# Kernel tuning notes

Hardware: AMD Instinct MI355X
Metric: run time of the kernel (lower is better)

Reference implementation:

```python
import jax, jax.numpy as jnp
import numpy as np

N_NODES = 50000
N_EDGES = 500000
HEADS = 4
OUT_CH = 64
POS_DIM = 16
IN_CH = 256
DIVERSITY_WEIGHT = 0.1
NEG_SLOPE = 0.2


def setup_inputs() -> dict:
    key = jax.random.key(0)
    k = jax.random.split(key, 6)
    x = jax.random.normal(k[0], (N_NODES, IN_CH + POS_DIM), dtype=jnp.float32)
    # edges with no self-loops by construction (col = row + nonzero offset mod N)
    row = jax.random.randint(k[1], (N_EDGES,), 0, N_NODES)
    off = jax.random.randint(k[2], (N_EDGES,), 1, N_NODES)
    col = (row + off) % N_NODES
    edge_index = jnp.stack([row, col]).astype(jnp.int64)
    lin_w = jax.random.normal(k[3], (HEADS * OUT_CH, IN_CH), dtype=jnp.float32) * (1.0 / np.sqrt(IN_CH))
    att = jax.random.normal(k[4], (1, HEADS, 2 * OUT_CH), dtype=jnp.float32) * 0.1
    pos_att = jax.random.normal(k[5], (1, HEADS, 2 * POS_DIM), dtype=jnp.float32) * 0.1
    bias = jnp.zeros((HEADS * OUT_CH,), dtype=jnp.float32)
    return {"x": x, "edge_index": edge_index, "lin_w": lin_w, "att": att,
            "pos_att": pos_att, "bias": bias}


def _forward(x, edge_index, lin_w, att, pos_att, bias):
    N = x.shape[0]
    H, C = HEADS, OUT_CH
    pos = x[:, -POS_DIM:]              # [N, P]
    content_feat = x[:, :-POS_DIM]     # [N, IN_CH]
    content = (content_feat @ lin_w.T).reshape(N, H, C)  # [N, H, C]

    # add self loops (input edges contain none)
    sl = jnp.arange(N)
    row = jnp.concatenate([edge_index[0], sl])  # [E+N]
    col = jnp.concatenate([edge_index[1], sl])

    # cat([x_i, x_j]) * att summed == per-node split logits, gathered per edge
    a_src = jnp.einsum('nhc,hc->nh', content, att[0, :, :C])   # [N, H]
    a_dst = jnp.einsum('nhc,hc->nh', content, att[0, :, C:])
    p_src = pos @ pos_att[0, :, :POS_DIM].T                    # [N, H]
    p_dst = pos @ pos_att[0, :, POS_DIM:].T

    alpha = a_src[row] + a_dst[col] + p_src[row] + p_dst[col]  # [E+N, H]
    alpha = jax.nn.leaky_relu(alpha, NEG_SLOPE)

    # segment softmax over destination node (row), PyG-style with +1e-16
    amax = jax.ops.segment_max(alpha, row, num_segments=N)
    alpha = jnp.exp(alpha - amax[row])
    denom = jax.ops.segment_sum(alpha, row, num_segments=N)
    alpha = alpha / (denom[row] + 1e-16)

    # attention-head diversity loss: pairwise cosine similarity of alpha columns
    norms = jnp.maximum(jnp.sqrt(jnp.sum(alpha * alpha, axis=0)), 1e-8)  # [H]
    an = alpha / norms
    corr = an.T @ an                                            # [H, H]
    corr = corr * (1.0 - jnp.eye(H, dtype=corr.dtype))          # zero diagonal
    diversity_loss = jnp.mean(corr) * DIVERSITY_WEIGHT

    msgs = content[col] * alpha[:, :, None]                     # [E+N, H, C]
    out = jax.ops.segment_sum(msgs, row, num_segments=N)        # [N, H, C]
    out = out.reshape(N, H * C) + bias
    return out, diversity_loss


def reference(x, edge_index, lin_w, att, pos_att, bias):
    return _forward(x, edge_index, lin_w, att, pos_att, bias)
```

## Files before the change

### kernel.cpp

```cpp
#include <hip/hip_runtime.h>
#include <math.h>

#define NN 50000
#define NE 500000
#define HH 4
#define CC 64
#define HC 256
#define PD 16
#define XD 272
#define NEG 0.2f
#define SB 1024
#define NBLK (NN / 4)

typedef _Float16 half4 __attribute__((ext_vector_type(4)));
typedef _Float16 half8 __attribute__((ext_vector_type(8)));
typedef float floatx4 __attribute__((ext_vector_type(4)));

__global__ void k_prep(const float* __restrict__ w, _Float16* __restrict__ wfrag,
                       int* __restrict__ counts, int* __restrict__ gcur) {
    int idx = blockIdx.x * blockDim.x + threadIdx.x;
    if (idx < NN) counts[idx] = 0;
    if (idx == NN) *gcur = 0;
    int j = idx & 7, lane = (idx >> 3) & 63, nt = (idx >> 9) & 3;
    int wv = (idx >> 11) & 3, kt = idx >> 13;
    int n = wv * 64 + nt * 16 + (lane & 15);
    int k = kt * 32 + (lane >> 4) * 8 + j;
    wfrag[idx] = (_Float16)w[(size_t)n * 256 + k];
}

__global__ __launch_bounds__(256) void k_gemm(const float* __restrict__ x,
                                              const _Float16* __restrict__ wfrag,
                                              const float* __restrict__ att,
                                              const float* __restrict__ patt,
                                              _Float16* __restrict__ content,
                                              float* __restrict__ ssrc,
                                              float* __restrict__ sdst) {
    const int tid = threadIdx.x;
    const int wv = tid >> 6, lane = tid & 63;
    const int nb = blockIdx.x * 64;
    const int m16 = lane & 15, q = lane >> 4;

    floatx4 acc[4][4];
#pragma unroll
    for (int mt = 0; mt < 4; mt++)
#pragma unroll
        for (int nt = 0; nt < 4; nt++) acc[mt][nt] = (floatx4){0.f, 0.f, 0.f, 0.f};

    const float* xr[4];
#pragma unroll
    for (int mt = 0; mt < 4; mt++) {
        int node = nb + mt * 16 + m16;
        if (node >= NN) node = NN - 1;
        xr[mt] = &x[(size_t)node * XD + q * 8];
    }

#pragma unroll
    for (int kt = 0; kt < 8; kt++) {
        half8 bf[4];
#pragma unroll
        for (int nt = 0; nt < 4; nt++)
            bf[nt] = *(const half8*)&wfrag[((((size_t)kt * 4 + wv) * 4 + nt) * 64 + lane) * 8];
        half8 af[4];
#pragma unroll
        for (int mt = 0; mt < 4; mt++) {
            float4 f0 = *(const float4*)(xr[mt] + kt * 32);
            float4 f1 = *(const float4*)(xr[mt] + kt * 32 + 4);
            half8 hv;
            hv[0] = (_Float16)f0.x; hv[1] = (_Float16)f0.y;
            hv[2] = (_Float16)f0.z; hv[3] = (_Float16)f0.w;
            hv[4] = (_Float16)f1.x; hv[5] = (_Float16)f1.y;
            hv[6] = (_Float16)f1.z; hv[7] = (_Float16)f1.w;
            af[mt] = hv;
        }
#pragma unroll
        for (int mt = 0; mt < 4; mt++)
#pragma unroll
            for (int nt = 0; nt < 4; nt++)
                acc[mt][nt] = __builtin_amdgcn_mfma_f32_16x16x32_f16(
                    af[mt], bf[nt], acc[mt][nt], 0, 0, 0);
    }

    const int h = wv;
#pragma unroll
    for (int mt = 0; mt < 4; mt++) {
#pragma unroll
        for (int r = 0; r < 4; r++) {
            int node = nb + mt * 16 + q * 4 + r;
            if (node < NN) {
                float sa = 0.f, sb = 0.f;
#pragma unroll
                for (int nt = 0; nt < 4; nt++) {
                    float v = acc[mt][nt][r];
                    int cih = nt * 16 + m16;
                    content[(size_t)node * 256 + h * 64 + cih] = (_Float16)v;
                    sa += v * att[h * 128 + cih];
                    sb += v * att[h * 128 + 64 + cih];
                }
                float pv = x[(size_t)node * XD + 256 + m16];
                sa += pv * patt[h * 32 + m16];
                sb += pv * patt[h * 32 + 16 + m16];
#pragma unroll
                for (int m = 1; m < 16; m <<= 1) {
                    sa += __shfl_xor(sa, m, 64);
                    sb += __shfl_xor(sb, m, 64);
                }
                if (m16 == 0) {
                    ssrc[node * 4 + h] = sa;
                    sdst[node * 4 + h] = sb;
                }
            }
        }
    }
}

__global__ void k_count(const int* __restrict__ row, int* __restrict__ counts,
                        int* __restrict__ slot) {
    int e = blockIdx.x * blockDim.x + threadIdx.x;
    if (e < NE) slot[e] = atomicAdd(&counts[row[e]], 1);
}

__global__ __launch_bounds__(SB) void k_offs(const int* __restrict__ counts,
                                             int* __restrict__ offs,
                                             int* __restrict__ gcur) {
    __shared__ int s[SB];
    __shared__ int basesh;
    int i = blockIdx.x * SB + threadIdx.x;
    int v = (i < NN) ? counts[i] : 0;
    s[threadIdx.x] = v;
    __syncthreads();
    for (int off = 1; off < SB; off <<= 1) {
        int t = (threadIdx.x >= off) ? s[threadIdx.x - off] : 0;
        __syncthreads();
        s[threadIdx.x] += t;
        __syncthreads();
    }
    if (threadIdx.x == SB - 1) basesh = atomicAdd(gcur, s[SB - 1]);
    __syncthreads();
    if (i < NN) offs[i] = basesh + s[threadIdx.x] - v;
}

__global__ void k_place(const int* __restrict__ row, const int* __restrict__ col,
                        const int* __restrict__ offs, const int* __restrict__ slot,
                        int* __restrict__ sorted) {
    int e = blockIdx.x * blockDim.x + threadIdx.x;
    if (e < NE) sorted[offs[row[e]] + slot[e]] = col[e];
}

__global__ __launch_bounds__(256) void k_node(const _Float16* __restrict__ content,
                                              const float* __restrict__ ssrc,
                                              const float* __restrict__ sdst,
                                              const int* __restrict__ counts,
                                              const int* __restrict__ off,
                                              const int* __restrict__ sorted,
                                              const float* __restrict__ bias,
                                              float* __restrict__ out,
                                              float* __restrict__ gpart) {
    __shared__ float gsh[16];
    __shared__ float ash[4][64][4];
    __shared__ int   csh[4][64];
    const int w = threadIdx.x >> 6;
    const int lane = threadIdx.x & 63;
    const int n = blockIdx.x * 4 + w;
    if (threadIdx.x < 16) gsh[threadIdx.x] = 0.f;
    __syncthreads();

    const int cnt = counts[n], base = off[n];
    const int total = cnt + 1;
    const float4 ss = *(const float4*)&ssrc[n * 4];
    const int hsel = lane >> 4;
    const half4* c4 = (const half4*)content;

    float4 acc = make_float4(0.f, 0.f, 0.f, 0.f);
    float g[10];
#pragma unroll
    for (int k = 0; k < 10; k++) g[k] = 0.f;

    if (total <= 64) {
        const int l = lane;
        const bool act = (l < total);
        const int c = (l < cnt) ? sorted[base + l] : n;
        float4 sd = *(const float4*)&sdst[c * 4];
        float r0 = ss.x + sd.x; r0 = r0 > 0.f ? r0 : NEG * r0;
        float r1 = ss.y + sd.y; r1 = r1 > 0.f ? r1 : NEG * r1;
        float r2 = ss.z + sd.z; r2 = r2 > 0.f ? r2 : NEG * r2;
        float r3 = ss.w + sd.w; r3 = r3 > 0.f ? r3 : NEG * r3;
        float m0 = act ? r0 : -1e30f, m1 = act ? r1 : -1e30f;
        float m2 = act ? r2 : -1e30f, m3 = act ? r3 : -1e30f;
#pragma unroll
        for (int s = 1; s < 64; s <<= 1) {
            m0 = fmaxf(m0, __shfl_xor(m0, s));
            m1 = fmaxf(m1, __shfl_xor(m1, s));
            m2 = fmaxf(m2, __shfl_xor(m2, s));
            m3 = fmaxf(m3, __shfl_xor(m3, s));
        }
        float e0 = act ? __expf(r0 - m0) : 0.f;
        float e1 = act ? __expf(r1 - m1) : 0.f;
        float e2 = act ? __expf(r2 - m2) : 0.f;
        float e3 = act ? __expf(r3 - m3) : 0.f;
        float s0 = e0, s1 = e1, s2 = e2, s3 = e3;
#pragma unroll
        for (int s = 1; s < 64; s <<= 1) {
            s0 += __shfl_xor(s0, s); s1 += __shfl_xor(s1, s);
            s2 += __shfl_xor(s2, s); s3 += __shfl_xor(s3, s);
        }
        float a0 = e0 / (s0 + 1e-16f), a1 = e1 / (s1 + 1e-16f);
        float a2 = e2 / (s2 + 1e-16f), a3 = e3 / (s3 + 1e-16f);

        g[0] = a0 * a0; g[1] = a0 * a1; g[2] = a0 * a2; g[3] = a0 * a3;
        g[4] = a1 * a1; g[5] = a1 * a2; g[6] = a1 * a3;
        g[7] = a2 * a2; g[8] = a2 * a3; g[9] = a3 * a3;

        ash[w][l][0] = a0; ash[w][l][1] = a1;
        ash[w][l][2] = a2; ash[w][l][3] = a3;
        csh[w][l] = c;

        const int nit = (total + 7) & ~7;
        for (int e = 0; e < nit; e += 8) {
            int   ci[8];
            float bi[8];
#pragma unroll
            for (int u = 0; u < 8; u++) {
                ci[u] = csh[w][e + u];
                bi[u] = ash[w][e + u][hsel];
            }
            half4 vi[8];
#pragma unroll
            for (int u = 0; u < 8; u++) vi[u] = c4[(size_t)ci[u] * 64 + lane];
#pragma unroll
            for (int u = 0; u < 8; u++) {
                acc.x += bi[u] * (float)vi[u][0];
                acc.y += bi[u] * (float)vi[u][1];
                acc.z += bi[u] * (float)vi[u][2];
                acc.w += bi[u] * (float)vi[u][3];
            }
        }
    } else {
        const int nch = (total + 63) >> 6;
        float m0 = -1e30f, m1 = -1e30f, m2 = -1e30f, m3 = -1e30f;
        for (int ch = 0; ch < nch; ch++) {
            int l = ch * 64 + lane;
            if (l < total) {
                int c = (l < cnt) ? sorted[base + l] : n;
                float4 sd = *(const float4*)&sdst[c * 4];
                float r0 = ss.x + sd.x; r0 = r0 > 0.f ? r0 : NEG * r0;
                float r1 = ss.y + sd.y; r1 = r1 > 0.f ? r1 : NEG * r1;
                float r2 = ss.z + sd.z; r2 = r2 > 0.f ? r2 : NEG * r2;
                float r3 = ss.w + sd.w; r3 = r3 > 0.f ? r3 : NEG * r3;
                m0 = fmaxf(m0, r0); m1 = fmaxf(m1, r1);
                m2 = fmaxf(m2, r2); m3 = fmaxf(m3, r3);
            }
        }
#pragma unroll
        for (int s = 1; s < 64; s <<= 1) {
            m0 = fmaxf(m0, __shfl_xor(m0, s));
            m1 = fmaxf(m1, __shfl_xor(m1, s));
            m2 = fmaxf(m2, __shfl_xor(m2, s));
            m3 = fmaxf(m3, __shfl_xor(m3, s));
        }
        float s0 = 0.f, s1 = 0.f, s2 = 0.f, s3 = 0.f;
        for (int ch = 0; ch < nch; ch++) {
            int l = ch * 64 + lane;
            if (l < total) {
                int c = (l < cnt) ? sorted[base + l] : n;
                float4 sd = *(const float4*)&sdst[c * 4];
                float r0 = ss.x + sd.x; r0 = r0 > 0.f ? r0 : NEG * r0;
                float r1 = ss.y + sd.y; r1 = r1 > 0.f ? r1 : NEG * r1;
                float r2 = ss.z + sd.z; r2 = r2 > 0.f ? r2 : NEG * r2;
                float r3 = ss.w + sd.w; r3 = r3 > 0.f ? r3 : NEG * r3;
                s0 += __expf(r0 - m0); s1 += __expf(r1 - m1);
                s2 += __expf(r2 - m2); s3 += __expf(r3 - m3);
            }
        }
#pragma unroll
        for (int s = 1; s < 64; s <<= 1) {
            s0 += __shfl_xor(s0, s); s1 += __shfl_xor(s1, s);
            s2 += __shfl_xor(s2, s); s3 += __shfl_xor(s3, s);
        }
        const float i0 = 1.f / (s0 + 1e-16f), i1 = 1.f / (s1 + 1e-16f);
        const float i2 = 1.f / (s2 + 1e-16f), i3 = 1.f / (s3 + 1e-16f);

        for (int ch = 0; ch < nch; ch++) {
            int l = ch * 64 + lane;
            int c = n;
            float a0 = 0.f, a1 = 0.f, a2 = 0.f, a3 = 0.f;
            if (l < total) {
                c = (l < cnt) ? sorted[base + l] : n;
                float4 sd = *(const float4*)&sdst[c * 4];
                float r0 = ss.x + sd.x; r0 = r0 > 0.f ? r0 : NEG * r0;
                float r1 = ss.y + sd.y; r1 = r1 > 0.f ? r1 : NEG * r1;
                float r2 = ss.z + sd.z; r2 = r2 > 0.f ? r2 : NEG * r2;
                float r3 = ss.w + sd.w; r3 = r3 > 0.f ? r3 : NEG * r3;
                a0 = __expf(r0 - m0) * i0; a1 = __expf(r1 - m1) * i1;
                a2 = __expf(r2 - m2) * i2; a3 = __expf(r3 - m3) * i3;
            }
            g[0] += a0 * a0; g[1] += a0 * a1; g[2] += a0 * a2; g[3] += a0 * a3;
            g[4] += a1 * a1; g[5] += a1 * a2; g[6] += a1 * a3;
            g[7] += a2 * a2; g[8] += a2 * a3; g[9] += a3 * a3;

            int cc = min(64, total - ch * 64);
            for (int e = 0; e < cc; e++) {
                float b0 = __shfl(a0, e), b1 = __shfl(a1, e);
                float b2 = __shfl(a2, e), b3 = __shfl(a3, e);
                int ce = __shfl(c, e);
                float mya = hsel == 0 ? b0 : hsel == 1 ? b1 : hsel == 2 ? b2 : b3;
                half4 cv = c4[(size_t)ce * 64 + lane];
                acc.x += mya * (float)cv[0]; acc.y += mya * (float)cv[1];
                acc.z += mya * (float)cv[2]; acc.w += mya * (float)cv[3];
            }
        }
    }

    float4 bv = ((const float4*)bias)[lane];
    acc.x += bv.x; acc.y += bv.y; acc.z += bv.z; acc.w += bv.w;
    ((float4*)out)[(size_t)n * 64 + lane] = acc;

#pragma unroll
    for (int s = 1; s < 64; s <<= 1) {
#pragma unroll
        for (int k = 0; k < 10; k++) g[k] += __shfl_xor(g[k], s);
    }
    if (lane == 0) {
#pragma unroll
        for (int k = 0; k < 10; k++) atomicAdd(&gsh[k], g[k]);
    }
    __syncthreads();
    if (threadIdx.x < 10) gpart[(size_t)blockIdx.x * 10 + threadIdx.x] = gsh[threadIdx.x];
}

__global__ __launch_bounds__(1024) void k_final(const float* __restrict__ gpart,
                                                float* __restrict__ out_div) {
    __shared__ float s[1024];
    const int t = threadIdx.x;
    const int k = t & 15, grp = t >> 4;
    float v = 0.f;
    if (k < 10) {
        for (int b = grp; b < NBLK; b += 64) v += gpart[(size_t)b * 10 + k];
    }
    s[t] = v;
    __syncthreads();
    for (int off = 512; off >= 16; off >>= 1) {
        if (t < off) s[t] += s[t + off];
        __syncthreads();
    }
    if (t == 0) {
        float g00 = s[0], g01 = s[1], g02 = s[2], g03 = s[3];
        float g11 = s[4], g12 = s[5], g13 = s[6];
        float g22 = s[7], g23 = s[8], g33 = s[9];
        float n0 = fmaxf(sqrtf(g00), 1e-8f), n1 = fmaxf(sqrtf(g11), 1e-8f);
        float n2 = fmaxf(sqrtf(g22), 1e-8f), n3 = fmaxf(sqrtf(g33), 1e-8f);
        float sum = g01 / (n0 * n1) + g02 / (n0 * n2) + g03 / (n0 * n3) +
                    g12 / (n1 * n2) + g13 / (n1 * n3) + g23 / (n2 * n3);
        sum *= 2.0f;
        out_div[0] = sum / 16.0f * 0.1f;
    }
}

extern "C" void kernel_launch(void* const* d_in, const int* in_sizes, int n_in,
                              void* d_out, int out_size, void* d_ws, size_t ws_size,
                              hipStream_t stream) {
    const float* x    = (const float*)d_in[0];
    const int*   ei   = (const int*)d_in[1];
    const int*   row  = ei;
    const int*   col  = ei + NE;
    const float* w    = (const float*)d_in[2];
    const float* att  = (const float*)d_in[3];
    const float* patt = (const float*)d_in[4];
    const float* bias = (const float*)d_in[5];
    float* out = (float*)d_out;

    char* p = (char*)d_ws;
    _Float16* content = (_Float16*)p; p += (size_t)NN * 256 * 2;
    _Float16* wfrag   = (_Float16*)p; p += (size_t)256 * 256 * 2;
    float* ssrc    = (float*)p; p += (size_t)NN * 4 * 4;
    float* sdst    = (float*)p; p += (size_t)NN * 4 * 4;
    float* gpart   = (float*)p; p += (size_t)NBLK * 10 * 4;
    int* counts    = (int*)p;   p += (size_t)NN * 4;
    int* offs      = (int*)p;   p += (size_t)NN * 4;
    int* gcur      = (int*)p;   p += 64;
    int* slot      = (int*)p;   p += (size_t)NE * 4;
    int* sorted    = (int*)p;   p += (size_t)NE * 4;

    k_prep<<<256, 256, 0, stream>>>(w, wfrag, counts, gcur);

    k_count<<<(NE + 255) / 256, 256, 0, stream>>>(row, counts, slot);

    k_gemm<<<(NN + 63) / 64, 256, 0, stream>>>(x, wfrag, att, patt, content, ssrc, sdst);

    int nb1 = (NN + SB - 1) / SB;
    k_offs<<<nb1, SB, 0, stream>>>(counts, offs, gcur);
    k_place<<<(NE + 255) / 256, 256, 0, stream>>>(row, col, offs, slot, sorted);

    k_node<<<NBLK, 256, 0, stream>>>(content, ssrc, sdst, counts, offs, sorted,
                                     bias, out, gpart);
    k_final<<<1, 1024, 0, stream>>>(gpart, out + (size_t)NN * 256);
}
```

Measured before the change: 305.3 us.

## Stage x tile in LDS as fp16 for GEMM; transpose attention weights for vector LDS reads

The GEMM kernel now loads the 64-row x tile once with coalesced reads, converts it to fp16 into shared memory, and feeds MFMA A-fragments from LDS. Previously every wave re-read and re-converted the same x rows from global memory. The node aggregation kernel stores per-edge attention weights head-major, so each lane fetches 8 weights and 8 column indices with vector LDS loads. Costs are extra LDS use (about 35KB per block), which may lower occupancy, plus a barrier and a changed summation order.

```diff
diff --git a/kernel.cpp b/kernel.cpp
--- a/kernel.cpp
+++ b/kernel.cpp
@@ -16,6 +16,8 @@
 typedef _Float16 half8 __attribute__((ext_vector_type(8)));
 typedef float floatx4 __attribute__((ext_vector_type(4)));
 
+#define ASTR 272
+
 __global__ void k_prep(const float* __restrict__ w, _Float16* __restrict__ wfrag,
                        int* __restrict__ counts, int* __restrict__ gcur) {
     int idx = blockIdx.x * blockDim.x + threadIdx.x;
@@ -35,43 +37,47 @@
                                               _Float16* __restrict__ content,
                                               float* __restrict__ ssrc,
                                               float* __restrict__ sdst) {
+    __shared__ _Float16 As[64 * ASTR];
     const int tid = threadIdx.x;
     const int wv = tid >> 6, lane = tid & 63;
     const int nb = blockIdx.x * 64;
     const int m16 = lane & 15, q = lane >> 4;
 
-    floatx4 acc[4][4];
-#pragma unroll
-    for (int mt = 0; mt < 4; mt++)
-#pragma unroll
-        for (int nt = 0; nt < 4; nt++) acc[mt][nt] = (floatx4){0.f, 0.f, 0.f, 0.f};
-
-    const float* xr[4];
-#pragma unroll
-    for (int mt = 0; mt < 4; mt++) {
-        int node = nb + mt * 16 + m16;
-        if (node >= NN) node = NN - 1;
-        xr[mt] = &x[(size_t)node * XD + q * 8];
-    }
-
-#pragma unroll
-    for (int kt = 0; kt < 8; kt++) {
-        half8 bf[4];
-#pragma unroll
-        for (int nt = 0; nt < 4; nt++)
-            bf[nt] = *(const half8*)&wfrag[((((size_t)kt * 4 + wv) * 4 + nt) * 64 + lane) * 8];
-        half8 af[4];
-#pragma unroll
-        for (int mt = 0; mt < 4; mt++) {
-            float4 f0 = *(const float4*)(xr[mt] + kt * 32);
-            float4 f1 = *(const float4*)(xr[mt] + kt * 32 + 4);
+    {
+        const int row = tid >> 2, kb = (tid & 3) * 64;
+        int node = nb + row; if (node >= NN) node = NN - 1;
+        const float* xp = &x[(size_t)node * XD + kb];
+        _Float16* ap = &As[row * ASTR + kb];
+#pragma unroll
+        for (int i = 0; i < 8; i++) {
+            float4 f0 = *(const float4*)(xp + i * 8);
+            float4 f1 = *(const float4*)(xp + i * 8 + 4);
             half8 hv;
             hv[0] = (_Float16)f0.x; hv[1] = (_Float16)f0.y;
             hv[2] = (_Float16)f0.z; hv[3] = (_Float16)f0.w;
             hv[4] = (_Float16)f1.x; hv[5] = (_Float16)f1.y;
             hv[6] = (_Float16)f1.z; hv[7] = (_Float16)f1.w;
-            af[mt] = hv;
-        }
+            *(half8*)(ap + i * 8) = hv;
+        }
+    }
+    __syncthreads();
+
+    floatx4 acc[4][4];
+#pragma unroll
+    for (int mt = 0; mt < 4; mt++)
+#pragma unroll
+        for (int nt = 0; nt < 4; nt++) acc[mt][nt] = (floatx4){0.f, 0.f, 0.f, 0.f};
+
+#pragma unroll
+    for (int kt = 0; kt < 8; kt++) {
+        half8 bf[4];
+#pragma unroll
+        for (int nt = 0; nt < 4; nt++)
+            bf[nt] = *(const half8*)&wfrag[((((size_t)kt * 4 + wv) * 4 + nt) * 64 + lane) * 8];
+        half8 af[4];
+#pragma unroll
+        for (int mt = 0; mt < 4; mt++)
+            af[mt] = *(half8*)&As[(mt * 16 + m16) * ASTR + kt * 32 + q * 8];
 #pragma unroll
         for (int mt = 0; mt < 4; mt++)
 #pragma unroll
@@ -156,7 +162,7 @@
                                               float* __restrict__ out,
                                               float* __restrict__ gpart) {
     __shared__ float gsh[16];
-    __shared__ float ash[4][64][4];
+    __shared__ float ashT[4][4][64];
     __shared__ int   csh[4][64];
     const int w = threadIdx.x >> 6;
     const int lane = threadIdx.x & 63;
@@ -210,29 +216,32 @@
         g[4] = a1 * a1; g[5] = a1 * a2; g[6] = a1 * a3;
         g[7] = a2 * a2; g[8] = a2 * a3; g[9] = a3 * a3;
 
-        ash[w][l][0] = a0; ash[w][l][1] = a1;
-        ash[w][l][2] = a2; ash[w][l][3] = a3;
+        ashT[w][0][l] = a0; ashT[w][1][l] = a1;
+        ashT[w][2][l] = a2; ashT[w][3][l] = a3;
         csh[w][l] = c;
 
         const int nit = (total + 7) & ~7;
         for (int e = 0; e < nit; e += 8) {
-            int   ci[8];
-            float bi[8];
-#pragma unroll
-            for (int u = 0; u < 8; u++) {
-                ci[u] = csh[w][e + u];
-                bi[u] = ash[w][e + u][hsel];
-            }
-            half4 vi[8];
-#pragma unroll
-            for (int u = 0; u < 8; u++) vi[u] = c4[(size_t)ci[u] * 64 + lane];
-#pragma unroll
-            for (int u = 0; u < 8; u++) {
-                acc.x += bi[u] * (float)vi[u][0];
-                acc.y += bi[u] * (float)vi[u][1];
-                acc.z += bi[u] * (float)vi[u][2];
-                acc.w += bi[u] * (float)vi[u][3];
-            }
+            float4 ba = *(const float4*)&ashT[w][hsel][e];
+            float4 bb = *(const float4*)&ashT[w][hsel][e + 4];
+            int4 ca = *(const int4*)&csh[w][e];
+            int4 cb = *(const int4*)&csh[w][e + 4];
+            half4 v0 = c4[(size_t)ca.x * 64 + lane];
+            half4 v1 = c4[(size_t)ca.y * 64 + lane];
+            half4 v2 = c4[(size_t)ca.z * 64 + lane];
+            half4 v3 = c4[(size_t)ca.w * 64 + lane];
+            half4 v4 = c4[(size_t)cb.x * 64 + lane];
+            half4 v5 = c4[(size_t)cb.y * 64 + lane];
+            half4 v6 = c4[(size_t)cb.z * 64 + lane];
+            half4 v7 = c4[(size_t)cb.w * 64 + lane];
+            acc.x += ba.x * (float)v0[0] + ba.y * (float)v1[0] + ba.z * (float)v2[0] + ba.w * (float)v3[0]
+                   + bb.x * (float)v4[0] + bb.y * (float)v5[0] + bb.z * (float)v6[0] + bb.w * (float)v7[0];
+            acc.y += ba.x * (float)v0[1] + ba.y * (float)v1[1] + ba.z * (float)v2[1] + ba.w * (float)v3[1]
+                   + bb.x * (float)v4[1] + bb.y * (float)v5[1] + bb.z * (float)v6[1] + bb.w * (float)v7[1];
+            acc.z += ba.x * (float)v0[2] + ba.y * (float)v1[2] + ba.z * (float)v2[2] + ba.w * (float)v3[2]
+                   + bb.x * (float)v4[2] + bb.y * (float)v5[2] + bb.z * (float)v6[2] + bb.w * (float)v7[2];
+            acc.w += ba.x * (float)v0[3] + ba.y * (float)v1[3] + ba.z * (float)v2[3] + ba.w * (float)v3[3]
+                   + bb.x * (float)v4[3] + bb.y * (float)v5[3] + bb.z * (float)v6[3] + bb.w * (float)v7[3];
         }
     } else {
         const int nch = (total + 63) >> 6;
```

Measured after the change: 289.6 us. 1.05x faster.
